# Kernel optimization log

Hardware: AMD Instinct MI355X
Metric: run time of the kernel (lower is better)

The kernel has to match this reference:

```python
import jax, jax.numpy as jnp
import numpy as np


def setup_inputs() -> dict:
    key = jax.random.key(0)
    k1, k2, k3, k4 = jax.random.split(key, 4)
    B, T, D, H = 64, 256, 2048, 2048
    scale_w = 1.0 / np.sqrt(D)
    scale_h = 1.0 / np.sqrt(H)
    return {
        "x": jax.random.normal(k1, (B, T, D), dtype=jnp.float32),
        "W": jax.random.normal(k2, (D, H), dtype=jnp.float32) * scale_w,
        "Wh": jax.random.normal(k3, (H, H), dtype=jnp.float32) * scale_h,
        "b": jax.random.normal(k4, (H,), dtype=jnp.float32) * 0.01,
    }


def reference(x, W, Wh, b):
    """Elman RNN: h_t = tanh(x_t @ W + h_{t-1} @ Wh + b), h_0 = 0.
    return_sequences=False and activation=identity, so output is the final state.
    (The original computes step 0 with a zero state then loops t=1..T-1, which
    is exactly a scan over all T steps starting from h=0.)"""
    B, T, D = x.shape
    H = Wh.shape[0]
    # Precompute the input projection for all timesteps in one big GEMM.
    xw = jnp.einsum('btd,dh->tbh', x, W) + b  # [T, B, H]

    def step(h, xw_t):
        h = jnp.tanh(xw_t + h @ Wh)
        return h, None

    h0 = jnp.zeros((B, H), dtype=x.dtype)
    h_last, _ = jax.lax.scan(step, h0, xw)
    return h_last  # [B, H]
```

## Files before the change

### kernel.cpp

```cpp
#include <hip/hip_runtime.h>
#include <hip/hip_bf16.h>
#include <hip/hip_fp16.h>

typedef _Float16 f16;
typedef _Float16 f16x8 __attribute__((ext_vector_type(8)));
typedef float f32x4 __attribute__((ext_vector_type(4)));
typedef unsigned int u32;
typedef unsigned long long u64;

#define HB 2048
#define DD 2048
#define TT 256
#define BB 64

typedef const __attribute__((address_space(1))) u32 gu32;
typedef __attribute__((address_space(3))) u32 lu32;

__device__ __forceinline__ void gl_lds16(const void* g, void* l) {
    __builtin_amdgcn_global_load_lds((gu32*)g, (lu32*)l, 16, 0, 0);
}

#define LOADM_SC0(dst, ar)                                                    \
    asm volatile("global_load_dwordx4 %0, %8, off sc0\n\t"                    \
                 "global_load_dwordx4 %1, %8, off offset:64 sc0\n\t"          \
                 "global_load_dwordx4 %2, %8, off offset:128 sc0\n\t"         \
                 "global_load_dwordx4 %3, %8, off offset:192 sc0\n\t"         \
                 "global_load_dwordx4 %4, %8, off offset:256 sc0\n\t"         \
                 "global_load_dwordx4 %5, %8, off offset:320 sc0\n\t"         \
                 "global_load_dwordx4 %6, %8, off offset:384 sc0\n\t"         \
                 "global_load_dwordx4 %7, %8, off offset:448 sc0"             \
                 : "=&v"(dst[0]), "=&v"(dst[1]), "=&v"(dst[2]), "=&v"(dst[3]),\
                   "=&v"(dst[4]), "=&v"(dst[5]), "=&v"(dst[6]), "=&v"(dst[7]) \
                 : "v"(ar)                                                    \
                 : "memory")

#define VMCNT0 asm volatile("s_waitcnt vmcnt(0)" ::: "memory")

__device__ __forceinline__ u32 ld_flag_sc0(const u32* p) {
    u32 v;
    asm volatile("global_load_dword %0, %1, off sc0\n\ts_waitcnt vmcnt(0)"
                 : "=v"(v) : "v"(p) : "memory");
    return v;
}
__device__ __forceinline__ u32 ld_flag_sc1(const u32* p) {
    u32 v;
    asm volatile("global_load_dword %0, %1, off sc1\n\ts_waitcnt vmcnt(0)"
                 : "=v"(v) : "v"(p) : "memory");
    return v;
}

__global__ __launch_bounds__(256) void k_transpose_cvt(const float* __restrict__ src,
                                                       f16* __restrict__ dst) {
    __shared__ f16 tile[64][65];
    int bx = blockIdx.x * 64;
    int by = blockIdx.y * 64;
    int tx = threadIdx.x & 63;
    int ty = threadIdx.x >> 6;
#pragma unroll
    for (int r = ty; r < 64; r += 4)
        tile[r][tx] = (f16)src[(size_t)(by + r) * HB + bx + tx];
    __syncthreads();
#pragma unroll
    for (int r = ty; r < 64; r += 4)
        dst[(size_t)(bx + r) * HB + by + tx] = tile[tx][r];
}

__global__ __launch_bounds__(256) void k_cvt_x(const float* __restrict__ x,
                                               f16* __restrict__ a16) {
    int r = blockIdx.x;
    int d = threadIdx.x * 8;
    const float* src = x + ((size_t)(r & 63) * TT + (r >> 6)) * DD + d;
    float4 v0 = *(const float4*)src;
    float4 v1 = *(const float4*)(src + 4);
    f16x8 o = {(f16)v0.x, (f16)v0.y, (f16)v0.z, (f16)v0.w,
               (f16)v1.x, (f16)v1.y, (f16)v1.z, (f16)v1.w};
    *(f16x8*)(a16 + (size_t)r * DD + d) = o;
}

__global__ __launch_bounds__(256) void k_gemm_xw_lds(const f16* __restrict__ a16,
                                                     const f16* __restrict__ W16T,
                                                     const float* __restrict__ bias,
                                                     f16* __restrict__ xw16) {
    __shared__ f16 As[128 * 32];
    __shared__ f16 Bs[128 * 32];
    int tid = threadIdx.x;
    int lane = tid & 63, w = tid >> 6;
    int wr = w >> 1, wc = w & 1;
    int lr = lane & 15, kg = lane >> 4;
    int rowBase = blockIdx.y * 128;
    int colBase = blockIdx.x * 128;

    f32x4 acc[4][4] = {};

    int r0 = tid >> 2, c0 = ((tid & 3) ^ ((r0 >> 1) & 3)) * 8;
    int u1 = tid + 256;
    int r1 = u1 >> 2, c1 = ((u1 & 3) ^ ((r1 >> 1) & 3)) * 8;
    const f16* gA0 = a16 + (size_t)(rowBase + r0) * DD + c0;
    const f16* gA1 = a16 + (size_t)(rowBase + r1) * DD + c1;
    const f16* gB0 = W16T + (size_t)(colBase + r0) * DD + c0;
    const f16* gB1 = W16T + (size_t)(colBase + r1) * DD + c1;
    f16* lA0 = As + (size_t)(w * 64) * 8;
    f16* lA1 = As + (size_t)(256 + w * 64) * 8;
    f16* lB0 = Bs + (size_t)(w * 64) * 8;
    f16* lB1 = Bs + (size_t)(256 + w * 64) * 8;

    for (int kk = 0; kk < DD; kk += 32) {
        gl_lds16(gA0 + kk, lA0);
        gl_lds16(gA1 + kk, lA1);
        gl_lds16(gB0 + kk, lB0);
        gl_lds16(gB1 + kk, lB1);
        __syncthreads();

        f16x8 af[4], bf[4];
#pragma unroll
        for (int mi = 0; mi < 4; ++mi) {
            int row = wr * 64 + mi * 16 + lr;
            af[mi] = *(const f16x8*)(As + row * 32 + (kg ^ ((row >> 1) & 3)) * 8);
        }
#pragma unroll
        for (int ni = 0; ni < 4; ++ni) {
            int rowb = wc * 64 + ni * 16 + lr;
            bf[ni] = *(const f16x8*)(Bs + rowb * 32 + (kg ^ ((rowb >> 1) & 3)) * 8);
        }
#pragma unroll
        for (int mi = 0; mi < 4; ++mi)
#pragma unroll
            for (int ni = 0; ni < 4; ++ni)
                acc[mi][ni] = __builtin_amdgcn_mfma_f32_16x16x32_f16(af[mi], bf[ni],
                                                                     acc[mi][ni], 0, 0, 0);
        __syncthreads();
    }

#pragma unroll
    for (int mi = 0; mi < 4; ++mi)
#pragma unroll
        for (int ni = 0; ni < 4; ++ni) {
            int col = colBase + wc * 64 + ni * 16 + lr;
            float bv = bias[col];
#pragma unroll
            for (int j = 0; j < 4; ++j) {
                int row = rowBase + wr * 64 + mi * 16 + kg * 4 + j;
                xw16[(size_t)row * HB + col] = (f16)(acc[mi][ni][j] + bv);
            }
        }
}

__global__ __launch_bounds__(256) void k_gemm_xw_direct(const float* __restrict__ x,
                                                        const f16* __restrict__ W16T,
                                                        const float* __restrict__ bias,
                                                        f16* __restrict__ xw16) {
    int lane = threadIdx.x & 63;
    int w = threadIdx.x >> 6;
    int wr = w >> 1, wc = w & 1;
    int rowBase = blockIdx.y * 64 + wr * 32;
    int colBase = blockIdx.x * 64 + wc * 32;
    int lr = lane & 15;
    int kg = lane >> 4;

    f32x4 acc[2][2] = {};

    int r0 = rowBase + lr;
    int r1 = rowBase + 16 + lr;
    const float* xrow0 = x + ((size_t)(r0 & 63) * TT + (r0 >> 6)) * DD;
    const float* xrow1 = x + ((size_t)(r1 & 63) * TT + (r1 >> 6)) * DD;
    const f16* wrow0 = W16T + (size_t)(colBase + lr) * DD;
    const f16* wrow1 = W16T + (size_t)(colBase + 16 + lr) * DD;

    for (int kk = 0; kk < DD; kk += 32) {
        int k = kk + kg * 8;
        const float4* pa0 = reinterpret_cast<const float4*>(xrow0 + k);
        const float4* pa1 = reinterpret_cast<const float4*>(xrow1 + k);
        float4 a0l = pa0[0], a0h = pa0[1];
        float4 a1l = pa1[0], a1h = pa1[1];
        f16x8 a0 = {(f16)a0l.x, (f16)a0l.y, (f16)a0l.z, (f16)a0l.w,
                    (f16)a0h.x, (f16)a0h.y, (f16)a0h.z, (f16)a0h.w};
        f16x8 a1 = {(f16)a1l.x, (f16)a1l.y, (f16)a1l.z, (f16)a1l.w,
                    (f16)a1h.x, (f16)a1h.y, (f16)a1h.z, (f16)a1h.w};
        f16x8 b0 = *reinterpret_cast<const f16x8*>(wrow0 + k);
        f16x8 b1 = *reinterpret_cast<const f16x8*>(wrow1 + k);
        acc[0][0] = __builtin_amdgcn_mfma_f32_16x16x32_f16(a0, b0, acc[0][0], 0, 0, 0);
        acc[0][1] = __builtin_amdgcn_mfma_f32_16x16x32_f16(a0, b1, acc[0][1], 0, 0, 0);
        acc[1][0] = __builtin_amdgcn_mfma_f32_16x16x32_f16(a1, b0, acc[1][0], 0, 0, 0);
        acc[1][1] = __builtin_amdgcn_mfma_f32_16x16x32_f16(a1, b1, acc[1][1], 0, 0, 0);
    }

#pragma unroll
    for (int mi = 0; mi < 2; ++mi)
#pragma unroll
        for (int ni = 0; ni < 2; ++ni) {
            int col = colBase + ni * 16 + lr;
            float bv = bias[col];
#pragma unroll
            for (int j = 0; j < 4; ++j) {
                int row = rowBase + mi * 16 + kg * 4 + j;
                xw16[(size_t)row * HB + col] = (f16)(acc[mi][ni][j] + bv);
            }
        }
}

__global__ __launch_bounds__(128) void k_rnn_step(const f16* __restrict__ hin,
                                                  const f16* __restrict__ WhT,
                                                  const f16* __restrict__ xw_t,
                                                  f16* __restrict__ hout,
                                                  float* __restrict__ dout, int last,
                                                  int first) {
    int lane = threadIdx.x & 63;
    int w = threadIdx.x >> 6;
    int m0 = blockIdx.y * 32 + w * 16;
    int n0 = blockIdx.x * 16;
    int lr = lane & 15;
    int kg = lane >> 4;

    f32x4 acc = {};
    if (!first) {
        const f16* arow = hin + (size_t)(m0 + lr) * HB;
        const f16* brow = WhT + (size_t)(n0 + lr) * HB;
#pragma unroll 4
        for (int kk = 0; kk < HB; kk += 32) {
            int k = kk + kg * 8;
            f16x8 a = *reinterpret_cast<const f16x8*>(arow + k);
            f16x8 b = *reinterpret_cast<const f16x8*>(brow + k);
            acc = __builtin_amdgcn_mfma_f32_16x16x32_f16(a, b, acc, 0, 0, 0);
        }
    }

#pragma unroll
    for (int j = 0; j < 4; ++j) {
        int row = m0 + kg * 4 + j;
        int col = n0 + lr;
        float pre = acc[j] + (float)xw_t[(size_t)row * HB + col];
        float h = tanhf(pre);
        hout[(size_t)row * HB + col] = (f16)h;
        if (last) dout[(size_t)row * HB + col] = h;
    }
}

__global__ __launch_bounds__(512, 2) void k_rnn_persist(const f16* __restrict__ Wh16T,
                                                        const f16* __restrict__ xw16,
                                                        f16* __restrict__ hseq,
                                                        float* __restrict__ dout,
                                                        u32* __restrict__ bar) {
    __shared__ float red[2][8][8][68];
    int tid = threadIdx.x;
    int lane = tid & 63, w = tid >> 6;
    int lr = lane & 15, kg = lane >> 4;
    int g = blockIdx.x & 7;
    int j = blockIdx.x >> 3;
    int row0 = g * 8;
    int n0 = j * 64;

    f16x8 bfrag[4][8];
#pragma unroll
    for (int n = 0; n < 4; ++n) {
        const f16* brow = Wh16T + (size_t)(n0 + n * 16 + lr) * DD + w * 256 + kg * 8;
#pragma unroll
        for (int s = 0; s < 8; ++s) bfrag[n][s] = *(const f16x8*)(brow + s * 32);
    }

    int f_row = tid >> 4;
    int f_c = (tid & 15) * 4;

    const u32* myflag =
        bar + (size_t)((((((w << 2) | (lane >> 1)) << 3) | g) << 1) | (lane & 1)) * 16;
    u32* ourflag = bar + (size_t)(((u32)blockIdx.x << 1) | (w & 1)) * 16;

    for (int t = 0; t < TT; ++t) {
        u64 xwv = 0;
        if (tid < 128)
            xwv = *(const u64*)(xw16 + ((size_t)t * BB + row0 + f_row) * HB + n0 + f_c);

        f32x4 acc[4] = {};
        if (t > 0) {
            u32 tgt = (u32)t;
            u32 v = (lane < 8) ? ld_flag_sc0(myflag) : tgt;
            int tries = 0;
            while (!__all(v >= tgt)) {
                __builtin_amdgcn_s_sleep(1);
                if (lane < 8)
                    v = (++tries < 8) ? ld_flag_sc0(myflag) : ld_flag_sc1(myflag);
            }
            __builtin_amdgcn_sched_barrier(0);

            const f16* abase = hseq + ((size_t)(t - 1) * BB + row0 + (lr & 7)) * HB +
                               w * 256 + kg * 8;
            f16x8 hv[8];
            LOADM_SC0(hv, abase);
            VMCNT0;
            __builtin_amdgcn_sched_barrier(0);
            if (lr >= 8) {
#pragma unroll
                for (int s = 0; s < 8; ++s) hv[s] = (f16x8)(f16)0;
            }
#pragma unroll
            for (int s = 0; s < 8; ++s)
#pragma unroll
                for (int n = 0; n < 4; ++n)
                    acc[n] = __builtin_amdgcn_mfma_f32_16x16x32_f16(hv[s], bfrag[n][s],
                                                                    acc[n], 0, 0, 0);
        }

        if (kg < 2) {
#pragma unroll
            for (int n = 0; n < 4; ++n)
#pragma unroll
                for (int jj = 0; jj < 4; ++jj)
                    red[t & 1][w][kg * 4 + jj][n * 16 + lr] = acc[n][jj];
        }
        __syncthreads();

        if (tid < 128) {
            float4 sum = {0.f, 0.f, 0.f, 0.f};
#pragma unroll
            for (int ww = 0; ww < 8; ++ww) {
                float4 v = *(const float4*)&red[t & 1][ww][f_row][f_c];
                sum.x += v.x; sum.y += v.y; sum.z += v.z; sum.w += v.w;
            }
            union { u64 q; f16 h[4]; } xwu;
            xwu.q = xwv;
            float h0 = tanhf(sum.x + (float)xwu.h[0]);
            float h1 = tanhf(sum.y + (float)xwu.h[1]);
            float h2 = tanhf(sum.z + (float)xwu.h[2]);
            float h3 = tanhf(sum.w + (float)xwu.h[3]);

            if (t == TT - 1) {
                float4 o = {h0, h1, h2, h3};
                *(float4*)(dout + (size_t)(row0 + f_row) * HB + n0 + f_c) = o;
            } else {
                union { u64 q; f16 h[4]; } ho;
                ho.h[0] = (f16)h0; ho.h[1] = (f16)h1;
                ho.h[2] = (f16)h2; ho.h[3] = (f16)h3;
                u64* dst = (u64*)(hseq + ((size_t)t * BB + row0 + f_row) * HB + n0 + f_c);
                *(volatile u64*)dst = ho.q;
                VMCNT0;
                if ((tid & 63) == 0)
                    *(volatile u32*)ourflag = (u32)(t + 1);
                __hip_atomic_store(dst, ho.q, __ATOMIC_RELAXED,
                                   __HIP_MEMORY_SCOPE_AGENT);
                VMCNT0;
                if ((tid & 63) == 0)
                    __hip_atomic_store(ourflag, (u32)(t + 1), __ATOMIC_RELAXED,
                                       __HIP_MEMORY_SCOPE_AGENT);
            }
        }
    }
}

extern "C" void kernel_launch(void* const* d_in, const int* in_sizes, int n_in,
                              void* d_out, int out_size, void* d_ws, size_t ws_size,
                              hipStream_t stream) {
    const float* x = (const float*)d_in[0];
    const float* W = (const float*)d_in[1];
    const float* Wh = (const float*)d_in[2];
    const float* bias = (const float*)d_in[3];
    float* dout = (float*)d_out;

    char* ws = (char*)d_ws;
    const size_t SZ_WT = (size_t)HB * DD * 2;
    const size_t SZ_H = (size_t)BB * HB * 2;
    const size_t SZ_XW = (size_t)TT * BB * HB * 2;
    const size_t OFF_W = 0;
    const size_t OFF_WH = OFF_W + SZ_WT;
    const size_t OFF_H01 = OFF_WH + SZ_WT;
    const size_t OFF_BAR = OFF_H01 + 2 * SZ_H;
    const size_t OFF_XW = OFF_BAR + 65536;
    const size_t OFF_HSEQ = OFF_XW + SZ_XW;
    const size_t NEED_FULL = OFF_HSEQ + SZ_XW;

    f16* W16T = (f16*)(ws + OFF_W);
    f16* Wh16T = (f16*)(ws + OFF_WH);
    f16* h0 = (f16*)(ws + OFF_H01);
    f16* h1 = (f16*)(ws + OFF_H01 + SZ_H);
    u32* bar = (u32*)(ws + OFF_BAR);
    f16* xw16 = (f16*)(ws + OFF_XW);
    f16* hseq = (f16*)(ws + OFF_HSEQ);

    dim3 tgrid(32, 32);
    k_transpose_cvt<<<tgrid, 256, 0, stream>>>(W, W16T);
    k_transpose_cvt<<<tgrid, 256, 0, stream>>>(Wh, Wh16T);

    if (ws_size >= NEED_FULL) {
        f16* x16 = hseq;
        k_cvt_x<<<TT * BB, 256, 0, stream>>>(x, x16);
        k_gemm_xw_lds<<<dim3(HB / 128, TT * BB / 128), 256, 0, stream>>>(x16, W16T, bias, xw16);
        hipMemsetAsync(bar, 0, 65536, stream);
        k_rnn_persist<<<256, 512, 0, stream>>>(Wh16T, xw16, hseq, dout, bar);
    } else {
        k_gemm_xw_direct<<<dim3(HB / 64, TT * BB / 64), 256, 0, stream>>>(x, W16T, bias, xw16);
        f16* hb[2] = {h0, h1};
        for (int t = 0; t < TT; ++t) {
            const f16* xwt = xw16 + (size_t)t * BB * HB;
            k_rnn_step<<<dim3(128, 2), 128, 0, stream>>>(hb[t & 1], Wh16T, xwt,
                                                         hb[(t + 1) & 1], dout,
                                                         t == TT - 1, t == 0);
        }
    }
}
```

Baseline: 1.470 ms.

## Spread epilogue over all eight waves with per-wave flags and split MFMA wait

The persistent RNN step kernel now has all eight waves each finalize one row of the 8x64 output tile, instead of only two waves handling four elements per lane. Each wave publishes its own flag, so consumers poll 32 flags per lane group instead of 8, and the barrier region grows to 256 KB. The h-load wait is split so the first four MFMA k-slices can start while the last four loads are still in flight. This spreads the tanh and store work across all waves and overlaps load latency with compute, at the cost of more flag polling traffic and narrower 16-bit stores.

Result: slower. 1.775 ms (+20.7%).

```diff
diff --git a/kernel.cpp b/kernel.cpp
--- a/kernel.cpp
+++ b/kernel.cpp
@@ -6,6 +6,7 @@
 typedef _Float16 f16x8 __attribute__((ext_vector_type(8)));
 typedef float f32x4 __attribute__((ext_vector_type(4)));
 typedef unsigned int u32;
+typedef unsigned short u16;
 typedef unsigned long long u64;
 
 #define HB 2048
@@ -35,6 +36,7 @@
                  : "memory")
 
 #define VMCNT0 asm volatile("s_waitcnt vmcnt(0)" ::: "memory")
+#define VMCNT4 asm volatile("s_waitcnt vmcnt(4)" ::: "memory")
 
 __device__ __forceinline__ u32 ld_flag_sc0(const u32* p) {
     u32 v;
@@ -47,6 +49,9 @@
     asm volatile("global_load_dword %0, %1, off sc1\n\ts_waitcnt vmcnt(0)"
                  : "=v"(v) : "v"(p) : "memory");
     return v;
+}
+__device__ __forceinline__ void st_u16_sc1(void* p, u16 v) {
+    asm volatile("global_store_short %0, %1, off sc1" :: "v"(p), "v"(v) : "memory");
 }
 
 __global__ __launch_bounds__(256) void k_transpose_cvt(const float* __restrict__ src,
@@ -257,26 +262,22 @@
         for (int s = 0; s < 8; ++s) bfrag[n][s] = *(const f16x8*)(brow + s * 32);
     }
 
-    int f_row = tid >> 4;
-    int f_c = (tid & 15) * 4;
-
+    int p_ = (lane >> 3) & 3;
     const u32* myflag =
-        bar + (size_t)((((((w << 2) | (lane >> 1)) << 3) | g) << 1) | (lane & 1)) * 16;
-    u32* ourflag = bar + (size_t)(((u32)blockIdx.x << 1) | (w & 1)) * 16;
+        bar + (size_t)((((u32)(4 * w + p_) * 8 + g) * 8) + (lane & 7)) * 16;
+    u32* ourflag = bar + (size_t)((u32)blockIdx.x * 8 + w) * 16;
 
     for (int t = 0; t < TT; ++t) {
-        u64 xwv = 0;
-        if (tid < 128)
-            xwv = *(const u64*)(xw16 + ((size_t)t * BB + row0 + f_row) * HB + n0 + f_c);
+        f16 xwv = xw16[((size_t)t * BB + row0 + w) * HB + n0 + lane];
 
         f32x4 acc[4] = {};
         if (t > 0) {
             u32 tgt = (u32)t;
-            u32 v = (lane < 8) ? ld_flag_sc0(myflag) : tgt;
+            u32 v = (lane < 32) ? ld_flag_sc0(myflag) : tgt;
             int tries = 0;
             while (!__all(v >= tgt)) {
                 __builtin_amdgcn_s_sleep(1);
-                if (lane < 8)
+                if (lane < 32)
                     v = (++tries < 8) ? ld_flag_sc0(myflag) : ld_flag_sc1(myflag);
             }
             __builtin_amdgcn_sched_barrier(0);
@@ -285,14 +286,26 @@
                                w * 256 + kg * 8;
             f16x8 hv[8];
             LOADM_SC0(hv, abase);
+            VMCNT4;
+            __builtin_amdgcn_sched_barrier(0);
+            if (lr >= 8) {
+#pragma unroll
+                for (int s = 0; s < 4; ++s) hv[s] = (f16x8)(f16)0;
+            }
+#pragma unroll
+            for (int s = 0; s < 4; ++s)
+#pragma unroll
+                for (int n = 0; n < 4; ++n)
+                    acc[n] = __builtin_amdgcn_mfma_f32_16x16x32_f16(hv[s], bfrag[n][s],
+                                                                    acc[n], 0, 0, 0);
             VMCNT0;
             __builtin_amdgcn_sched_barrier(0);
             if (lr >= 8) {
 #pragma unroll
-                for (int s = 0; s < 8; ++s) hv[s] = (f16x8)(f16)0;
-            }
-#pragma unroll
-            for (int s = 0; s < 8; ++s)
+                for (int s = 4; s < 8; ++s) hv[s] = (f16x8)(f16)0;
+            }
+#pragma unroll
+            for (int s = 4; s < 8; ++s)
 #pragma unroll
                 for (int n = 0; n < 4; ++n)
                     acc[n] = __builtin_amdgcn_mfma_f32_16x16x32_f16(hv[s], bfrag[n][s],
@@ -308,36 +321,25 @@
         }
         __syncthreads();
 
-        if (tid < 128) {
-            float4 sum = {0.f, 0.f, 0.f, 0.f};
-#pragma unroll
-            for (int ww = 0; ww < 8; ++ww) {
-                float4 v = *(const float4*)&red[t & 1][ww][f_row][f_c];
-                sum.x += v.x; sum.y += v.y; sum.z += v.z; sum.w += v.w;
-            }
-            union { u64 q; f16 h[4]; } xwu;
-            xwu.q = xwv;
-            float h0 = tanhf(sum.x + (float)xwu.h[0]);
-            float h1 = tanhf(sum.y + (float)xwu.h[1]);
-            float h2 = tanhf(sum.z + (float)xwu.h[2]);
-            float h3 = tanhf(sum.w + (float)xwu.h[3]);
+        {
+            float sum = 0.f;
+#pragma unroll
+            for (int ww = 0; ww < 8; ++ww) sum += red[t & 1][ww][w][lane];
+            float h = tanhf(sum + (float)xwv);
 
             if (t == TT - 1) {
-                float4 o = {h0, h1, h2, h3};
-                *(float4*)(dout + (size_t)(row0 + f_row) * HB + n0 + f_c) = o;
+                dout[(size_t)(row0 + w) * HB + n0 + lane] = h;
             } else {
-                union { u64 q; f16 h[4]; } ho;
-                ho.h[0] = (f16)h0; ho.h[1] = (f16)h1;
-                ho.h[2] = (f16)h2; ho.h[3] = (f16)h3;
-                u64* dst = (u64*)(hseq + ((size_t)t * BB + row0 + f_row) * HB + n0 + f_c);
-                *(volatile u64*)dst = ho.q;
+                union { f16 f; u16 s; } hb;
+                hb.f = (f16)h;
+                f16* dst = hseq + ((size_t)t * BB + row0 + w) * HB + n0 + lane;
+                *(volatile u16*)dst = hb.s;
                 VMCNT0;
-                if ((tid & 63) == 0)
+                if (lane == 0)
                     *(volatile u32*)ourflag = (u32)(t + 1);
-                __hip_atomic_store(dst, ho.q, __ATOMIC_RELAXED,
-                                   __HIP_MEMORY_SCOPE_AGENT);
+                st_u16_sc1(dst, hb.s);
                 VMCNT0;
-                if ((tid & 63) == 0)
+                if (lane == 0)
                     __hip_atomic_store(ourflag, (u32)(t + 1), __ATOMIC_RELAXED,
                                        __HIP_MEMORY_SCOPE_AGENT);
             }
@@ -358,11 +360,12 @@
     const size_t SZ_WT = (size_t)HB * DD * 2;
     const size_t SZ_H = (size_t)BB * HB * 2;
     const size_t SZ_XW = (size_t)TT * BB * HB * 2;
+    const size_t SZ_BAR = 262144;
     const size_t OFF_W = 0;
     const size_t OFF_WH = OFF_W + SZ_WT;
     const size_t OFF_H01 = OFF_WH + SZ_WT;
     const size_t OFF_BAR = OFF_H01 + 2 * SZ_H;
-    const size_t OFF_XW = OFF_BAR + 65536;
+    const size_t OFF_XW = OFF_BAR + SZ_BAR;
     const size_t OFF_HSEQ = OFF_XW + SZ_XW;
     const size_t NEED_FULL = OFF_HSEQ + SZ_XW;
 
@@ -382,7 +385,7 @@
         f16* x16 = hseq;
         k_cvt_x<<<TT * BB, 256, 0, stream>>>(x, x16);
         k_gemm_xw_lds<<<dim3(HB / 128, TT * BB / 128), 256, 0, stream>>>(x16, W16T, bias, xw16);
-        hipMemsetAsync(bar, 0, 65536, stream);
+        hipMemsetAsync(bar, 0, SZ_BAR, stream);
         k_rnn_persist<<<256, 512, 0, stream>>>(Wh16T, xw16, hseq, dout, bar);
     } else {
         k_gemm_xw_direct<<<dim3(HB / 64, TT * BB / 64), 256, 0, stream>>>(x, W16T, bias, xw16);
```
